# Kernel tuning notes

Hardware: AMD Instinct MI355X
Metric: run time of the kernel (lower is better)

## Reference

```python
import jax, jax.numpy as jnp
import numpy as np

RANK = 32
NC = 32                      # n_components = out_features / rank = 1024/32
TRI = RANK * (RANK + 1) // 2  # 528
EPS = 1e-5


def setup_inputs() -> dict:
    key = jax.random.key(0)
    k1, k2, k3, k4, k5 = jax.random.split(key, 5)
    B, T, D = 2, 2048, 1024
    param_arg = jax.random.normal(k1, (B, T, D), dtype=jnp.float32)
    input_arg = jax.random.normal(k2, (B, T, D), dtype=jnp.float32)
    # learned params (weight_norm linears collapse to plain weight matrices)
    W_uv = jax.random.normal(k3, (NC * TRI, D), dtype=jnp.float32) * 0.02
    W_alpha = jax.random.normal(k4, (NC, D), dtype=jnp.float32) * 0.02
    b_alpha = jax.random.normal(k5, (NC,), dtype=jnp.float32) * 0.02
    return {"param_arg": param_arg, "input_arg": input_arg,
            "W_uv": W_uv, "W_alpha": W_alpha, "b_alpha": b_alpha}


def reference(param_arg, input_arg, W_uv, W_alpha, b_alpha):
    B, T, D = input_arg.shape
    N = B * T * NC
    # projections (mixer_ac = identity)
    params = jnp.einsum('btd,pd->btp', param_arg, W_uv)            # [B,T,NC*TRI]
    alpha = jax.nn.sigmoid(jnp.einsum('btd,cd->btc', param_arg, W_alpha) + b_alpha)  # [B,T,NC]
    p = params.reshape(N, TRI)
    iu, ju = jnp.triu_indices(RANK)
    uv = jnp.zeros((N, RANK, RANK), dtype=p.dtype).at[:, iu, ju].set(p)
    uv = jnp.einsum('nij,nkj->nik', uv, uv)                        # U U^T, symmetric PSD
    # per-column L2 norm (dim=-2), then max over columns
    col = jnp.sqrt(jnp.sum(uv * uv, axis=-2, keepdims=True))       # [N,1,RANK]
    uv = uv / (jnp.max(col, axis=-1, keepdims=True) + EPS)
    x = input_arg.reshape(N, RANK)                                 # (-1, rank, 1)
    y = alpha.reshape(N, 1) * jnp.einsum('nij,nj->ni', uv, x)      # [N,RANK]
    return input_arg - y.reshape(B, T, D)
```

## Files before the change

### kernel.cpp

```cpp
#include <hip/hip_runtime.h>
#include <hip/hip_bf16.h>
#include <stdint.h>

typedef float f32x4 __attribute__((ext_vector_type(4)));
typedef float f32x16 __attribute__((ext_vector_type(16)));
typedef __bf16 bf16x8 __attribute__((ext_vector_type(8)));

#define EPS 1e-5f

static __device__ __forceinline__ unsigned short f2bf(float f) {
  unsigned int u = __float_as_uint(f);
  unsigned int r = (u + 0x7fffu + ((u >> 16) & 1u)) >> 16;
  return (unsigned short)r;
}

static __device__ __forceinline__ void gload_lds16(const unsigned short* g, unsigned short* s) {
  __builtin_amdgcn_global_load_lds((const __attribute__((address_space(1))) unsigned int*)g,
                                   (__attribute__((address_space(3))) unsigned int*)s,
                                   16, 0, 0);
}

__global__ __launch_bounds__(256) void k_head(const float* __restrict__ Wsrc,
                                              unsigned short* __restrict__ Wb,
                                              const float* __restrict__ A,
                                              const float* __restrict__ Wa,
                                              const float* __restrict__ ba,
                                              float* __restrict__ alpha,
                                              unsigned short* __restrict__ Ab) {
  __shared__ __align__(16) float arow[1024];
  if (blockIdx.x < 4096) {
    const int n4 = (16896 * 1024) / 4;
    int idx = blockIdx.x * 256 + threadIdx.x;
    for (int i = idx; i < n4; i += 4096 * 256) {
      f32x4 v = ((const f32x4*)Wsrc)[i];
      ushort4 o;
      o.x = f2bf(v.x); o.y = f2bf(v.y); o.z = f2bf(v.z); o.w = f2bf(v.w);
      ((ushort4*)Wb)[i] = o;
    }
    return;
  }
  const int bt = blockIdx.x - 4096, tid = threadIdx.x;
  f32x4 v = ((const f32x4*)(A + (size_t)bt * 1024))[tid];
  ((f32x4*)arow)[tid] = v;
  ushort4 o;
  o.x = f2bf(v.x); o.y = f2bf(v.y); o.z = f2bf(v.z); o.w = f2bf(v.w);
  ((ushort4*)(Ab + (size_t)bt * 1024))[tid] = o;
  __syncthreads();
  const int c = tid >> 3, h = tid & 7;
  const float* wr = Wa + (size_t)c * 1024 + h * 128;
  const float* ar = arow + h * 128;
  float s = 0.f;
#pragma unroll 8
  for (int j = 0; j < 128; j += 4) {
    f32x4 wv = *(const f32x4*)(wr + j);
    s += wv.x * ar[j] + wv.y * ar[j + 1] + wv.z * ar[j + 2] + wv.w * ar[j + 3];
  }
  s += __shfl_down(s, 4);
  s += __shfl_down(s, 2);
  s += __shfl_down(s, 1);
  if (h == 0) {
    float z = s + ba[c];
    alpha[(size_t)bt * 32 + c] = 1.f / (1.f + __expf(-z));
  }
}


#define SWZ(b) ((b) ^ ((((b) >> 7) & 7) << 4))

#define STG(mat, off, ldsoff) \
  gload_lds16((const unsigned short*)((const char*)(mat) + (unsigned)(off)), \
              (unsigned short*)(smem + (ldsoff) + widK))

#define READ_A(p0, p1, qm) do {                                                 \
  _Pragma("unroll") for (int _mi = 0; _mi < 4; ++_mi) {                         \
    af[_mi][0] = *(const bf16x8*)((p0) + (qm) * 8192 + _mi * 2048);             \
    af[_mi][1] = *(const bf16x8*)((p1) + (qm) * 8192 + _mi * 2048);             \
  } } while (0)

#define READ_B(p0, p1, qn) do {                                                 \
  _Pragma("unroll") for (int _ni = 0; _ni < 2; ++_ni) {                         \
    bfr[qn][_ni][0] = *(const bf16x8*)((p0) + (qn) * 4096 + _ni * 2048);        \
    bfr[qn][_ni][1] = *(const bf16x8*)((p1) + (qn) * 4096 + _ni * 2048);        \
  } } while (0)

#define MMA(qm, qn) do {                                                        \
  __builtin_amdgcn_s_setprio(1);                                                \
  _Pragma("unroll") for (int _mi = 0; _mi < 4; ++_mi)                           \
  _Pragma("unroll") for (int _ni = 0; _ni < 2; ++_ni)                           \
  _Pragma("unroll") for (int _ks = 0; _ks < 2; ++_ks)                           \
    acc[(qm) * 4 + _mi][(qn) * 2 + _ni] = __builtin_amdgcn_mfma_f32_16x16x32_bf16( \
        af[_mi][_ks], bfr[qn][_ni][_ks], acc[(qm) * 4 + _mi][(qn) * 2 + _ni], 0, 0, 0); \
  __builtin_amdgcn_s_setprio(0);                                                \
  } while (0)

#define PH_SYNC do {                                                            \
  __builtin_amdgcn_s_barrier();                                                 \
  asm volatile("s_waitcnt lgkmcnt(0)" ::: "memory");                            \
  __builtin_amdgcn_sched_barrier(0);                                            \
  } while (0)

#define ENDBAR __builtin_amdgcn_s_barrier()
#define VMW6 asm volatile("s_waitcnt vmcnt(6)" ::: "memory")
#define VMW0 asm volatile("s_waitcnt vmcnt(0)" ::: "memory")
#define LGKM8 asm volatile("s_waitcnt lgkmcnt(8)" ::: "memory")

__global__ __launch_bounds__(512, 2) void k_gemm8(const unsigned short* __restrict__ A,
                                                  const unsigned short* __restrict__ W,
                                                  unsigned short* __restrict__ C) {
  extern __shared__ char smem[];
  const int bid = blockIdx.x;
  const int tm = bid / 66, tn = bid - tm * 66;
  const int m0 = tm << 8, n0 = tn << 8;
  const int tid = threadIdx.x;
  const int lane = tid & 63;
  const int wid = tid >> 6;
  const int wm = wid >> 2, wn = wid & 3;
  const int fr = lane & 15, fq = lane >> 4;
  const int widK = wid * 1024;

  const int sb0 = SWZ(tid * 16);
  const int sb1 = SWZ(8192 + tid * 16);
  const int oB0_0 = (n0 + (sb0 >> 7)) * 2048 + (sb0 & 127);
  const int oB0_1 = (n0 + (sb1 >> 7)) * 2048 + (sb1 & 127);
  const int oB1_0 = oB0_0 + 128 * 2048;
  const int oB1_1 = oB0_1 + 128 * 2048;
  const int oA0_0 = (m0 + (sb0 >> 7)) * 2048 + (sb0 & 127);
  const int oA0_1 = (m0 + (sb1 >> 7)) * 2048 + (sb1 & 127);
  const int oA1_0 = oA0_0 + 128 * 2048;
  const int oA1_1 = oA0_1 + 128 * 2048;

  const int lane0 = fr * 128 + ((fq ^ (fr & 7)) << 4);
  const int lane1 = fr * 128 + (((4 | fq) ^ (fr & 7)) << 4);
  char* const aK0b0 = smem + wm * 16384 + lane0;
  char* const aK1b0 = smem + wm * 16384 + lane1;
  char* const aK0b1 = aK0b0 + 65536;
  char* const aK1b1 = aK1b0 + 65536;
  char* const bb = smem + 32768 + (wn >> 1) * 16384 + (wn & 1) * 8192;
  char* const bK0b0 = bb + lane0;
  char* const bK1b0 = bb + lane1;
  char* const bK0b1 = bK0b0 + 65536;
  char* const bK1b1 = bK1b0 + 65536;

  f32x4 acc[8][4];
#pragma unroll
  for (int i = 0; i < 8; ++i)
#pragma unroll
    for (int j = 0; j < 4; ++j) acc[i][j] = (f32x4){0.f, 0.f, 0.f, 0.f};

  bf16x8 af[4][2];
  bf16x8 bfr[2][2][2];

  STG(W, oB0_0, 32768); STG(W, oB0_1, 40960);
  STG(W, oB1_0, 49152); STG(W, oB1_1, 57344);
  STG(A, oA0_0, 0);     STG(A, oA0_1, 8192);
  STG(A, oA1_0, 16384); STG(A, oA1_1, 24576);
  STG(W, oB0_0 + 128, 98304);  STG(W, oB0_1 + 128, 106496);
  STG(W, oB1_0 + 128, 114688); STG(W, oB1_1 + 128, 122880);
  STG(A, oA0_0 + 128, 65536);  STG(A, oA0_1 + 128, 73728);
  VMW6;
  __builtin_amdgcn_s_barrier();

  for (int i = 0; i < 8; ++i) {
    const int kb1 = 256 * i + 128, kb2 = kb1 + 128, kb3 = kb2 + 128;
    READ_A(aK0b0, aK1b0, 0); READ_B(bK0b0, bK1b0, 0);
    STG(A, oA1_0 + kb1, 81920); STG(A, oA1_1 + kb1, 90112);
    LGKM8;
    PH_SYNC; MMA(0, 0); ENDBAR;
    READ_B(bK0b0, bK1b0, 1);
    PH_SYNC; MMA(0, 1); ENDBAR;
    READ_A(aK0b0, aK1b0, 1);
    if (i < 7) { STG(W, oB0_0 + kb2, 32768); STG(W, oB0_1 + kb2, 40960); }
    PH_SYNC; MMA(1, 0); ENDBAR;
    if (i < 7) {
      STG(W, oB1_0 + kb2, 49152); STG(W, oB1_1 + kb2, 57344);
      STG(A, oA0_0 + kb2, 0);     STG(A, oA0_1 + kb2, 8192);
      VMW6;
    } else { VMW0; }
    PH_SYNC; MMA(1, 1); ENDBAR;
    READ_A(aK0b1, aK1b1, 0); READ_B(bK0b1, bK1b1, 0);
    if (i < 7) { STG(A, oA1_0 + kb2, 16384); STG(A, oA1_1 + kb2, 24576); }
    LGKM8;
    PH_SYNC; MMA(0, 0); ENDBAR;
    READ_B(bK0b1, bK1b1, 1);
    PH_SYNC; MMA(0, 1); ENDBAR;
    READ_A(aK0b1, aK1b1, 1);
    if (i < 7) { STG(W, oB0_0 + kb3, 98304); STG(W, oB0_1 + kb3, 106496); }
    PH_SYNC; MMA(1, 0); ENDBAR;
    if (i < 7) {
      STG(W, oB1_0 + kb3, 114688); STG(W, oB1_1 + kb3, 122880);
      STG(A, oA0_0 + kb3, 65536);  STG(A, oA0_1 + kb3, 73728);
      VMW6;
    }
    PH_SYNC; MMA(1, 1); ENDBAR;
  }

#pragma unroll
  for (int am = 0; am < 8; ++am)
#pragma unroll
    for (int an = 0; an < 4; ++an)
#pragma unroll
      for (int r = 0; r < 4; ++r) {
        int row = m0 + (wm << 7) + (am << 4) + (fq << 2) + r;
        int col = n0 + (wn << 6) + (an << 4) + fr;
        C[(size_t)row * 16896 + col] = f2bf(acc[am][an][r]);
      }
}

__global__ __launch_bounds__(256) void k_epi(const unsigned short* __restrict__ P,
                                             const float* __restrict__ X,
                                             const float* __restrict__ alpha,
                                             float* __restrict__ out) {
  __shared__ __align__(16) unsigned short U[4][1280];
  __shared__ __align__(16) float Xl[512];
  __shared__ unsigned short tab[528];
  const int tid = threadIdx.x;
  for (int e = tid; e < 528; e += 256) {
    float fi = (65.0f - sqrtf((float)(4225 - 8 * e))) * 0.5f;
    int i = (int)fi;
    int oi = (i * (65 - i)) >> 1;
    if (e < oi) { --i; oi = (i * (65 - i)) >> 1; }
    else { int oi1 = ((i + 1) * (64 - i)) >> 1; if (e >= oi1) { oi = oi1; ++i; } }
    tab[e] = (unsigned short)(i * 40 + i + (e - oi));
  }
  const int w = tid >> 6, lane = tid & 63;
  const int nblk = blockIdx.x << 4;
  const int btB = nblk >> 5, c0 = nblk & 31;
  if (tid < 128)
    ((f32x4*)Xl)[tid] = ((const f32x4*)(X + (size_t)btB * 1024 + c0 * 32))[tid];
  __syncthreads();

  unsigned short* Uw = U[w];
  const int col = lane & 31, hi = lane >> 5;

#pragma unroll
  for (int it = 0; it < 4; ++it) {
    const int li = (w << 2) + it;
    const int n = nblk + li;
    const int c = c0 + li;
#pragma unroll
    for (int t = 0; t < 5; ++t) ((ushort4*)Uw)[lane + (t << 6)] = make_ushort4(0, 0, 0, 0);
    const unsigned short* p = P + (size_t)btB * 16896 + c * 528;
#pragma unroll
    for (int e = 0; e < 9; ++e) {
      int idx = lane + (e << 6);
      if (idx < 528) Uw[tab[idx]] = p[idx];
    }
    bf16x8 fa0 = *(const bf16x8*)&Uw[col * 40 + (hi << 3)];
    bf16x8 fa1 = *(const bf16x8*)&Uw[col * 40 + 16 + (hi << 3)];
    f32x16 S = {0.f, 0.f, 0.f, 0.f, 0.f, 0.f, 0.f, 0.f,
                0.f, 0.f, 0.f, 0.f, 0.f, 0.f, 0.f, 0.f};
    S = __builtin_amdgcn_mfma_f32_32x32x16_bf16(fa0, fa0, S, 0, 0, 0);
    S = __builtin_amdgcn_mfma_f32_32x32x16_bf16(fa1, fa1, S, 0, 0, 0);

    float css = 0.f;
#pragma unroll
    for (int r = 0; r < 16; ++r) css += S[r] * S[r];
    css += __shfl_xor(css, 32);
    float m = css;
#pragma unroll
    for (int off = 1; off < 32; off <<= 1) m = fmaxf(m, __shfl_xor(m, off));
    m = sqrtf(m);
    const float scale = alpha[n] / (m + EPS);

    const float* xw = Xl + li * 32;
    f32x4 x0 = *(const f32x4*)&xw[(hi << 2)];
    f32x4 x1 = *(const f32x4*)&xw[8 + (hi << 2)];
    f32x4 x2 = *(const f32x4*)&xw[16 + (hi << 2)];
    f32x4 x3 = *(const f32x4*)&xw[24 + (hi << 2)];
    float y = 0.f;
#pragma unroll
    for (int r = 0; r < 4; ++r) y += x0[r] * S[r];
#pragma unroll
    for (int r = 0; r < 4; ++r) y += x1[r] * S[4 + r];
#pragma unroll
    for (int r = 0; r < 4; ++r) y += x2[r] * S[8 + r];
#pragma unroll
    for (int r = 0; r < 4; ++r) y += x3[r] * S[12 + r];
    y += __shfl_xor(y, 32);

    if (hi == 0) {
      out[(size_t)btB * 1024 + c * 32 + col] = xw[col] - scale * y;
    }
  }
}

extern "C" void kernel_launch(void* const* d_in, const int* in_sizes, int n_in,
                              void* d_out, int out_size, void* d_ws, size_t ws_size,
                              hipStream_t stream) {
  const float* param = (const float*)d_in[0];
  const float* input = (const float*)d_in[1];
  const float* W_uv  = (const float*)d_in[2];
  const float* W_al  = (const float*)d_in[3];
  const float* b_al  = (const float*)d_in[4];
  float* out = (float*)d_out;

  char* ws = (char*)d_ws;
  unsigned short* Ab    = (unsigned short*)(ws);
  unsigned short* Wb    = (unsigned short*)(ws + 8388608);
  float*          alpha = (float*)(ws + 42991616);
  unsigned short* Pp    = (unsigned short*)(ws + 43515904);

  (void)hipFuncSetAttribute((const void*)k_gemm8,
                            hipFuncAttributeMaxDynamicSharedMemorySize, 131072);

  k_head<<<8192, 256, 0, stream>>>(W_uv, Wb, param, W_al, b_al, alpha, Ab);
  k_gemm8<<<16 * 66, 512, 131072, stream>>>(Ab, Wb, Pp);
  k_epi<<<131072 / 16, 256, 0, stream>>>(Pp, input, alpha, out);
}
```

Measured before the change: 291.6 us.

## Restructure GEMM main loop into two phases per K-slab with whole-slab prefetch

Reorganizes the bf16 GEMM inner loop so each 128-wide K slab runs in two phases (upper and lower M halves) instead of four quadrant phases. That halves the number of barriers. All eight global-to-LDS loads for the next slab are issued in one group, and LDS reads are split so the MFMAs can start after a partial lgkmcnt wait. It replaces the staggered vmcnt(6) pipelining with a full vmcnt(0) wait before the second phase. This may expose global load latency in exchange for fewer synchronization points.

```diff
diff --git a/kernel.cpp b/kernel.cpp
--- a/kernel.cpp
+++ b/kernel.cpp
@@ -77,13 +77,19 @@
     af[_mi][1] = *(const bf16x8*)((p1) + (qm) * 8192 + _mi * 2048);             \
   } } while (0)
 
+#define READ_A2(p0, p1, qm, mlo) do {                                           \
+  _Pragma("unroll") for (int _mi = (mlo); _mi < (mlo) + 2; ++_mi) {             \
+    af[_mi][0] = *(const bf16x8*)((p0) + (qm) * 8192 + _mi * 2048);             \
+    af[_mi][1] = *(const bf16x8*)((p1) + (qm) * 8192 + _mi * 2048);             \
+  } } while (0)
+
 #define READ_B(p0, p1, qn) do {                                                 \
   _Pragma("unroll") for (int _ni = 0; _ni < 2; ++_ni) {                         \
     bfr[qn][_ni][0] = *(const bf16x8*)((p0) + (qn) * 4096 + _ni * 2048);        \
     bfr[qn][_ni][1] = *(const bf16x8*)((p1) + (qn) * 4096 + _ni * 2048);        \
   } } while (0)
 
-#define MMA(qm, qn) do {                                                        \
+#define MMAq(qm, qn) do {                                                       \
   __builtin_amdgcn_s_setprio(1);                                                \
   _Pragma("unroll") for (int _mi = 0; _mi < 4; ++_mi)                           \
   _Pragma("unroll") for (int _ni = 0; _ni < 2; ++_ni)                           \
@@ -93,16 +99,24 @@
   __builtin_amdgcn_s_setprio(0);                                                \
   } while (0)
 
-#define PH_SYNC do {                                                            \
-  __builtin_amdgcn_s_barrier();                                                 \
-  asm volatile("s_waitcnt lgkmcnt(0)" ::: "memory");                            \
-  __builtin_amdgcn_sched_barrier(0);                                            \
+#define MMAh(qm, mlo) do {                                                      \
+  __builtin_amdgcn_s_setprio(1);                                                \
+  _Pragma("unroll") for (int _mi = (mlo); _mi < (mlo) + 2; ++_mi)               \
+  _Pragma("unroll") for (int _qn = 0; _qn < 2; ++_qn)                           \
+  _Pragma("unroll") for (int _ni = 0; _ni < 2; ++_ni)                           \
+  _Pragma("unroll") for (int _ks = 0; _ks < 2; ++_ks)                           \
+    acc[(qm) * 4 + _mi][_qn * 2 + _ni] = __builtin_amdgcn_mfma_f32_16x16x32_bf16( \
+        af[_mi][_ks], bfr[_qn][_ni][_ks], acc[(qm) * 4 + _mi][_qn * 2 + _ni], 0, 0, 0); \
+  __builtin_amdgcn_s_setprio(0);                                                \
   } while (0)
 
+#define SB __builtin_amdgcn_sched_barrier(0)
+#define LG4 do { asm volatile("s_waitcnt lgkmcnt(4)" ::: "memory"); SB; } while (0)
+#define LG0 do { asm volatile("s_waitcnt lgkmcnt(0)" ::: "memory"); SB; } while (0)
 #define ENDBAR __builtin_amdgcn_s_barrier()
-#define VMW6 asm volatile("s_waitcnt vmcnt(6)" ::: "memory")
+#define PHBAR __builtin_amdgcn_s_barrier()
+#define VMW8 asm volatile("s_waitcnt vmcnt(8)" ::: "memory")
 #define VMW0 asm volatile("s_waitcnt vmcnt(0)" ::: "memory")
-#define LGKM8 asm volatile("s_waitcnt lgkmcnt(8)" ::: "memory")
 
 __global__ __launch_bounds__(512, 2) void k_gemm8(const unsigned short* __restrict__ A,
                                                   const unsigned short* __restrict__ W,
@@ -157,41 +171,55 @@
   STG(W, oB0_0 + 128, 98304);  STG(W, oB0_1 + 128, 106496);
   STG(W, oB1_0 + 128, 114688); STG(W, oB1_1 + 128, 122880);
   STG(A, oA0_0 + 128, 65536);  STG(A, oA0_1 + 128, 73728);
-  VMW6;
+  STG(A, oA1_0 + 128, 81920);  STG(A, oA1_1 + 128, 90112);
+  VMW8;
   __builtin_amdgcn_s_barrier();
 
   for (int i = 0; i < 8; ++i) {
-    const int kb1 = 256 * i + 128, kb2 = kb1 + 128, kb3 = kb2 + 128;
-    READ_A(aK0b0, aK1b0, 0); READ_B(bK0b0, bK1b0, 0);
-    STG(A, oA1_0 + kb1, 81920); STG(A, oA1_1 + kb1, 90112);
-    LGKM8;
-    PH_SYNC; MMA(0, 0); ENDBAR;
+    const int kbO = (2 * i + 1) * 128;
+    const int kbE = (2 * i + 2) * 128;
+    READ_B(bK0b0, bK1b0, 0); READ_A(aK0b0, aK1b0, 0);
+    SB;
     READ_B(bK0b0, bK1b0, 1);
-    PH_SYNC; MMA(0, 1); ENDBAR;
-    READ_A(aK0b0, aK1b0, 1);
-    if (i < 7) { STG(W, oB0_0 + kb2, 32768); STG(W, oB0_1 + kb2, 40960); }
-    PH_SYNC; MMA(1, 0); ENDBAR;
+    if (i >= 1) {
+      STG(W, oB0_0 + kbO, 98304);  STG(W, oB0_1 + kbO, 106496);
+      STG(W, oB1_0 + kbO, 114688); STG(W, oB1_1 + kbO, 122880);
+      STG(A, oA0_0 + kbO, 65536);  STG(A, oA0_1 + kbO, 73728);
+      STG(A, oA1_0 + kbO, 81920);  STG(A, oA1_1 + kbO, 90112);
+    }
+    PHBAR;
+    LG4; MMAq(0, 0);
+    LG0; MMAq(0, 1);
+    ENDBAR;
+    READ_A2(aK0b0, aK1b0, 1, 0);
+    SB;
+    READ_A2(aK0b0, aK1b0, 1, 2);
+    VMW0;
+    PHBAR;
+    LG4; MMAh(1, 0);
+    LG0; MMAh(1, 2);
+    ENDBAR;
+    READ_B(bK0b1, bK1b1, 0); READ_A(aK0b1, aK1b1, 0);
+    SB;
+    READ_B(bK0b1, bK1b1, 1);
     if (i < 7) {
-      STG(W, oB1_0 + kb2, 49152); STG(W, oB1_1 + kb2, 57344);
-      STG(A, oA0_0 + kb2, 0);     STG(A, oA0_1 + kb2, 8192);
-      VMW6;
-    } else { VMW0; }
-    PH_SYNC; MMA(1, 1); ENDBAR;
-    READ_A(aK0b1, aK1b1, 0); READ_B(bK0b1, bK1b1, 0);
-    if (i < 7) { STG(A, oA1_0 + kb2, 16384); STG(A, oA1_1 + kb2, 24576); }
-    LGKM8;
-    PH_SYNC; MMA(0, 0); ENDBAR;
-    READ_B(bK0b1, bK1b1, 1);
-    PH_SYNC; MMA(0, 1); ENDBAR;
-    READ_A(aK0b1, aK1b1, 1);
-    if (i < 7) { STG(W, oB0_0 + kb3, 98304); STG(W, oB0_1 + kb3, 106496); }
-    PH_SYNC; MMA(1, 0); ENDBAR;
-    if (i < 7) {
-      STG(W, oB1_0 + kb3, 114688); STG(W, oB1_1 + kb3, 122880);
-      STG(A, oA0_0 + kb3, 65536);  STG(A, oA0_1 + kb3, 73728);
-      VMW6;
-    }
-    PH_SYNC; MMA(1, 1); ENDBAR;
+      STG(W, oB0_0 + kbE, 32768); STG(W, oB0_1 + kbE, 40960);
+      STG(W, oB1_0 + kbE, 49152); STG(W, oB1_1 + kbE, 57344);
+      STG(A, oA0_0 + kbE, 0);     STG(A, oA0_1 + kbE, 8192);
+      STG(A, oA1_0 + kbE, 16384); STG(A, oA1_1 + kbE, 24576);
+    }
+    PHBAR;
+    LG4; MMAq(0, 0);
+    LG0; MMAq(0, 1);
+    ENDBAR;
+    READ_A2(aK0b1, aK1b1, 1, 0);
+    SB;
+    READ_A2(aK0b1, aK1b1, 1, 2);
+    VMW0;
+    PHBAR;
+    LG4; MMAh(1, 0);
+    LG0; MMAh(1, 2);
+    ENDBAR;
   }
 
 #pragma unroll
```

Result: slower. 301.0 us (+3.2%).
